# Performance work log

Measured on AMD Instinct MI355X. Metric: run time of the kernel, lower is better.

## Reference

```python
import jax, jax.numpy as jnp
import numpy as np

N = 10000   # nodes
E = 80000   # edges per graph (avg degree 8)
H = 32      # hidden width (hard-coded in module)
VD0 = 2048  # visual_dim for gcn_0
VD1 = 256   # visual_dim // 8 for gcn_b21


def setup_inputs() -> dict:
    key = jax.random.key(0)
    ks = jax.random.split(key, 16)
    rn = lambda k, s, sc=1.0: jax.random.normal(k, s, dtype=jnp.float32) * sc
    return {
        "x": rn(ks[0], (N, 9)),
        "vis0": rn(ks[1], (N, VD0)),
        "vis1": rn(ks[2], (N, VD1)),
        "edge_index0": jax.random.randint(ks[3], (2, E), 0, N),
        "edge_index1": jax.random.randint(ks[4], (2, E), 0, N),
        # input_mlp: Linear(9,32) -> BatchNorm1d(32) (eval) -> PReLU -> Dropout(0) -> Linear(32,32)
        "W_in1": rn(ks[5], (9, H), 0.3), "b_in1": jnp.zeros((H,), jnp.float32),
        "bn_gamma": jnp.ones((H,), jnp.float32), "bn_beta": jnp.zeros((H,), jnp.float32),
        "bn_mean": jnp.zeros((H,), jnp.float32), "bn_var": jnp.ones((H,), jnp.float32),
        "prelu_a": jnp.asarray(0.25, jnp.float32),
        "W_in2": rn(ks[6], (H, H), 0.15), "b_in2": jnp.zeros((H,), jnp.float32),
        "w_node": rn(ks[7], (H, 1), 0.15), "b_node": jnp.zeros((1,), jnp.float32),
        "W_c0": rn(ks[8], (H, H), 0.15), "b_c0": jnp.zeros((H,), jnp.float32),
        "W_c1": rn(ks[9], (H, H), 0.15), "b_c1": jnp.zeros((H,), jnp.float32),
        "w_p0": rn(ks[10], (H, 1), 0.15), "b_p0": jnp.zeros((1,), jnp.float32),
        "w_p1": rn(ks[11], (H, 1), 0.15), "b_p1": jnp.zeros((1,), jnp.float32),
    }


def _cm_cos_conv(h, edge_index, vis, W, b):
    # gather-weight-scatter: w_e = cos(vis[src], vis[dst]); out_i = (sum_e->i w_e * h[src_e]) @ W + b
    src, dst = edge_index[0], edge_index[1]
    vn = vis * jax.lax.rsqrt(jnp.sum(vis * vis, axis=-1, keepdims=True) + 1e-8)
    w = jnp.sum(vn[src] * vn[dst], axis=-1)  # [E] cosine similarity per edge
    agg = jax.ops.segment_sum(h[src] * w[:, None], dst, num_segments=h.shape[0])  # [N,H]
    return agg @ W + b  # conv_activation=None -> identity


def reference(x, vis0, vis1, edge_index0, edge_index1, W_in1, b_in1, bn_gamma, bn_beta, bn_mean, bn_var, prelu_a, W_in2, b_in2, w_node, b_node, W_c0, b_c0, W_c1, b_c1, w_p0, b_p0, w_p1, b_p1):
    h = x @ W_in1 + b_in1
    h = bn_gamma * (h - bn_mean) * jax.lax.rsqrt(bn_var + 1e-5) + bn_beta
    h = jnp.where(h >= 0, h, prelu_a * h)  # PReLU (single shared slope)
    h = h @ W_in2 + b_in2                   # [N,32] shared for graphs 0 and 4
    nodes_scores = (h @ w_node + b_node)[:, 0]
    h0 = _cm_cos_conv(h, edge_index0, vis0, W_c0, b_c0)
    h1 = _cm_cos_conv(h, edge_index1, vis1, W_c1, b_c1)
    s0 = (h0 @ w_p0 + b_p0)[:, 0]
    s1 = (h1 @ w_p1 + b_p1)[:, 0]
    return nodes_scores + s0 + s1
```

## Files before the change

### kernel.cpp

```cpp
#include <hip/hip_runtime.h>

#define N_NODES 10000
#define NE      80000
#define H       32
#define VD0     2048
#define VD1     256

#define EDGE_CAP 32

#define S_BLOCKS 313
#define A_MLP    40
#define A_NC0    2500
#define A_NC1    2500
#define PREP_BLOCKS (S_BLOCKS + A_MLP + A_NC0 + A_NC1)

#define E0_BLOCKS 5000
#define E1_BLOCKS 2500
#define OVF_BLOCKS 16
#define EDGE_BLOCKS (E0_BLOCKS + E1_BLOCKS + OVF_BLOCKS)

__device__ inline int dot4i8(unsigned a, unsigned b, int c) {
#if __has_builtin(__builtin_amdgcn_sdot4)
    return __builtin_amdgcn_sdot4((int)a, (int)b, c, false);
#else
    int s = c;
    s += ((int)(a << 24) >> 24) * ((int)(b << 24) >> 24);
    s += ((int)(a << 16) >> 24) * ((int)(b << 16) >> 24);
    s += ((int)(a <<  8) >> 24) * ((int)(b <<  8) >> 24);
    s += ((int)a >> 24)         * ((int)b >> 24);
    return s;
#endif
}
__device__ inline int dot16i8(uint4 a, uint4 b, int c) {
    c = dot4i8(a.x, b.x, c);
    c = dot4i8(a.y, b.y, c);
    c = dot4i8(a.z, b.z, c);
    c = dot4i8(a.w, b.w, c);
    return c;
}

struct KP {
    const float* x;
    const float* vis0; const float* vis1;
    const int* ei0; const int* ei1;
    const float* W_in1; const float* b_in1;
    const float* bn_gamma; const float* bn_beta;
    const float* bn_mean; const float* bn_var;
    const float* prelu_a;
    const float* W_in2; const float* b_in2;
    const float* w_node; const float* b_node;
    const float* W_c0; const float* b_c0;
    const float* W_c1; const float* b_c1;
    const float* w_p0; const float* b_p0;
    const float* w_p1; const float* b_p1;
    float* out; float* p0w; float* p1w;
    signed char* vn0; signed char* vn1;
    float* s00; float* s01;
    uint2* b0; uint2* b1;
    int2* ovf0; int2* ovf1;
    int* cur0; int* cur1; int* ovfn;
};

template <int VD>
__device__ inline void normconv_q_node(const float* __restrict__ vis,
                                       signed char* __restrict__ vn,
                                       float* __restrict__ s0,
                                       int node, int lane)
{
    const float4* v = (const float4*)(vis + (size_t)node * VD);
    float4 f[VD / 256];
    float acc = 0.f, amax = 0.f;
    #pragma unroll
    for (int it = 0; it < VD / 256; it++) {
        f[it] = v[it * 64 + lane];
        acc += f[it].x * f[it].x + f[it].y * f[it].y
             + f[it].z * f[it].z + f[it].w * f[it].w;
        float m = fmaxf(fmaxf(fabsf(f[it].x), fabsf(f[it].y)),
                        fmaxf(fabsf(f[it].z), fabsf(f[it].w)));
        amax = fmaxf(amax, m);
    }
    #pragma unroll
    for (int o = 32; o; o >>= 1) {
        acc  += __shfl_xor(acc, o);
        amax  = fmaxf(amax, __shfl_xor(amax, o));
    }
    const float inv  = rsqrtf(acc + 1e-8f);
    const float vmax = amax * inv;
    const float k    = vmax > 0.f ? inv * (127.f / vmax) : 0.f;
    if (lane == 0) s0[node] = vmax * (1.f / 127.f);
    uint* o4 = (uint*)(vn + (size_t)node * VD);
    #pragma unroll
    for (int it = 0; it < VD / 256; it++) {
        const int q0 = (int)rintf(f[it].x * k);
        const int q1 = (int)rintf(f[it].y * k);
        const int q2 = (int)rintf(f[it].z * k);
        const int q3 = (int)rintf(f[it].w * k);
        o4[it * 64 + lane] = (unsigned)(q0 & 0xff)
                           | ((unsigned)(q1 & 0xff) << 8)
                           | ((unsigned)(q2 & 0xff) << 16)
                           | ((unsigned)(q3 & 0xff) << 24);
    }
}

__device__ inline void stageA_unit(const KP& p, int u, int t)
{
    if (u < A_MLP) {
        __shared__ float sW1[9 * H];
        __shared__ float sW2[H * H];
        __shared__ float sU0[H], sU1[H], sWn[H];
        __shared__ float sB1[H], sB2[H], sSc[H], sSh[H];
        __shared__ float sC;

        for (int i = t; i < 9 * H; i += 256) sW1[i] = p.W_in1[i];
        for (int i = t; i < H * H; i += 256) sW2[i] = p.W_in2[i];
        if (t < H) {
            sB1[t] = p.b_in1[t];
            sB2[t] = p.b_in2[t];
            float sc = p.bn_gamma[t] * rsqrtf(p.bn_var[t] + 1e-5f);
            sSc[t] = sc;
            sSh[t] = p.bn_beta[t] - p.bn_mean[t] * sc;
            sWn[t] = p.w_node[t];
            float u0 = 0.f, u1 = 0.f;
            for (int j = 0; j < H; j++) {
                u0 += p.W_c0[t * H + j] * p.w_p0[j];
                u1 += p.W_c1[t * H + j] * p.w_p1[j];
            }
            sU0[t] = u0; sU1[t] = u1;
        }
        if (t == 0) {
            float c0 = p.b_p0[0], c1 = p.b_p1[0];
            for (int j = 0; j < H; j++) { c0 += p.b_c0[j] * p.w_p0[j]; c1 += p.b_c1[j] * p.w_p1[j]; }
            sC = c0 + c1 + p.b_node[0];
        }
        __syncthreads();

        const float a = p.prelu_a[0];
        const int n = u * 256 + t;
        if (n < N_NODES) {
            float xi[9];
            #pragma unroll
            for (int i = 0; i < 9; i++) xi[i] = p.x[n * 9 + i];

            float tt[H];
            #pragma unroll
            for (int j = 0; j < H; j++) {
                float s = sB1[j];
                #pragma unroll
                for (int i = 0; i < 9; i++) s += xi[i] * sW1[i * H + j];
                s = s * sSc[j] + sSh[j];
                tt[j] = s >= 0.f ? s : a * s;
            }

            float ns = 0.f, p0 = 0.f, p1 = 0.f;
            #pragma unroll
            for (int k = 0; k < H; k++) {
                float h = sB2[k];
                #pragma unroll
                for (int j = 0; j < H; j++) h += tt[j] * sW2[j * H + k];
                ns += h * sWn[k];
                p0 += h * sU0[k];
                p1 += h * sU1[k];
            }
            p.out[n] = ns + sC;
            p.p0w[n] = p0;
            p.p1w[n] = p1;
        }
    } else if (u < A_MLP + A_NC0) {
        const int node = (u - A_MLP) * 4 + (t >> 6);
        normconv_q_node<VD0>(p.vis0, p.vn0, p.s00, node, t & 63);
    } else {
        const int node = (u - A_MLP - A_NC0) * 4 + (t >> 6);
        normconv_q_node<VD1>(p.vis1, p.vn1, p.s01, node, t & 63);
    }
}

__device__ inline void stageB_edge(const KP& p, int e)
{
    {
        const int s = p.ei0[e];
        const int d = p.ei0[NE + e];
        const int pos = atomicAdd(&p.cur0[d], 1);
        if (pos < EDGE_CAP)
            p.b0[d * EDGE_CAP + pos] = make_uint2((unsigned)(s * VD0), (unsigned)s);
        else
            p.ovf0[atomicAdd(&p.ovfn[0], 1)] = make_int2(d, s);
    }
    {
        const int s = p.ei1[e];
        const int d = p.ei1[NE + e];
        const int pos = atomicAdd(&p.cur1[d], 1);
        if (pos < EDGE_CAP)
            p.b1[d * EDGE_CAP + pos] = make_uint2((unsigned)(s * VD1), (unsigned)s);
        else
            p.ovf1[atomicAdd(&p.ovfn[1], 1)] = make_int2(d, s);
    }
}

__global__ __launch_bounds__(256) void edge4_kernel(KP p)
{
    const int bid  = blockIdx.x;
    const int t    = threadIdx.x;
    const int lane = t & 63;
    const int warp = t >> 6;

    if (bid < E0_BLOCKS) {
        const int phase = bid & 1;
        const int d     = (bid >> 1) * 4 + warp;
        int cnt = p.cur0[d];
        if (cnt <= 0) return;
        cnt = cnt < EDGE_CAP ? cnt : EDGE_CAP;

        const char* base = (const char*)p.vn0;
        const int koffB  = phase * 1024 + lane * 16;
        const uint4 dreg = *(const uint4*)(base + (size_t)d * VD0 + koffB);
        const uint2* eb  = p.b0 + (size_t)d * EDGE_CAP;

        float partial = 0.f;
        int j = 0;
        for (; j + 3 < cnt; j += 4) {
            const uint2 e0 = eb[j], e1 = eb[j + 1], e2 = eb[j + 2], e3 = eb[j + 3];
            const uint4 r0 = *(const uint4*)(base + e0.x + koffB);
            const uint4 r1 = *(const uint4*)(base + e1.x + koffB);
            const uint4 r2 = *(const uint4*)(base + e2.x + koffB);
            const uint4 r3 = *(const uint4*)(base + e3.x + koffB);
            const float w0 = p.p0w[e0.y] * p.s00[e0.y];
            const float w1 = p.p0w[e1.y] * p.s00[e1.y];
            const float w2 = p.p0w[e2.y] * p.s00[e2.y];
            const float w3 = p.p0w[e3.y] * p.s00[e3.y];
            partial += (float)dot16i8(dreg, r0, 0) * w0;
            partial += (float)dot16i8(dreg, r1, 0) * w1;
            partial += (float)dot16i8(dreg, r2, 0) * w2;
            partial += (float)dot16i8(dreg, r3, 0) * w3;
        }
        for (; j < cnt; j++) {
            const uint2 e0 = eb[j];
            const uint4 r0 = *(const uint4*)(base + e0.x + koffB);
            partial += (float)dot16i8(dreg, r0, 0) * (p.p0w[e0.y] * p.s00[e0.y]);
        }
        #pragma unroll
        for (int o = 32; o; o >>= 1) partial += __shfl_down(partial, o);
        if (lane == 0) atomicAdd(&p.out[d], partial * p.s00[d]);
    } else if (bid < E0_BLOCKS + E1_BLOCKS) {
        const int d = (bid - E0_BLOCKS) * 4 + warp;
        int cnt = p.cur1[d];
        if (cnt <= 0) return;
        cnt = cnt < EDGE_CAP ? cnt : EDGE_CAP;

        const char* base = (const char*)p.vn1;
        const int koffB  = lane * 4;
        const unsigned dreg = *(const unsigned*)(base + (size_t)d * VD1 + koffB);
        const uint2* eb  = p.b1 + (size_t)d * EDGE_CAP;

        float partial = 0.f;
        int j = 0;
        for (; j + 3 < cnt; j += 4) {
            const uint2 e0 = eb[j], e1 = eb[j + 1], e2 = eb[j + 2], e3 = eb[j + 3];
            const unsigned r0 = *(const unsigned*)(base + e0.x + koffB);
            const unsigned r1 = *(const unsigned*)(base + e1.x + koffB);
            const unsigned r2 = *(const unsigned*)(base + e2.x + koffB);
            const unsigned r3 = *(const unsigned*)(base + e3.x + koffB);
            const float w0 = p.p1w[e0.y] * p.s01[e0.y];
            const float w1 = p.p1w[e1.y] * p.s01[e1.y];
            const float w2 = p.p1w[e2.y] * p.s01[e2.y];
            const float w3 = p.p1w[e3.y] * p.s01[e3.y];
            partial += (float)dot4i8(dreg, r0, 0) * w0;
            partial += (float)dot4i8(dreg, r1, 0) * w1;
            partial += (float)dot4i8(dreg, r2, 0) * w2;
            partial += (float)dot4i8(dreg, r3, 0) * w3;
        }
        for (; j < cnt; j++) {
            const uint2 e0 = eb[j];
            const unsigned r0 = *(const unsigned*)(base + e0.x + koffB);
            partial += (float)dot4i8(dreg, r0, 0) * (p.p1w[e0.y] * p.s01[e0.y]);
        }
        #pragma unroll
        for (int o = 32; o; o >>= 1) partial += __shfl_down(partial, o);
        if (lane == 0) atomicAdd(&p.out[d], partial * p.s01[d]);
    } else {
        const int wv = (bid - E0_BLOCKS - E1_BLOCKS) * 4 + warp;
        const int n0 = p.ovfn[0];
        for (int i = wv; i < n0; i += OVF_BLOCKS * 4) {
            const int2 ds = p.ovf0[i];
            const uint4* A = (const uint4*)(p.vn0 + (size_t)ds.y * VD0);
            const uint4* B = (const uint4*)(p.vn0 + (size_t)ds.x * VD0);
            int id = 0;
            id = dot16i8(A[lane * 2],     B[lane * 2],     id);
            id = dot16i8(A[lane * 2 + 1], B[lane * 2 + 1], id);
            float acc = (float)id;
            #pragma unroll
            for (int o = 32; o; o >>= 1) acc += __shfl_down(acc, o);
            if (lane == 0)
                atomicAdd(&p.out[ds.x],
                          acc * p.s00[ds.y] * p.s00[ds.x] * p.p0w[ds.y]);
        }
        const int n1 = p.ovfn[1];
        for (int i = wv; i < n1; i += OVF_BLOCKS * 4) {
            const int2 ds = p.ovf1[i];
            const unsigned* A = (const unsigned*)(p.vn1 + (size_t)ds.y * VD1);
            const unsigned* B = (const unsigned*)(p.vn1 + (size_t)ds.x * VD1);
            float acc = (float)dot4i8(A[lane], B[lane], 0);
            #pragma unroll
            for (int o = 32; o; o >>= 1) acc += __shfl_down(acc, o);
            if (lane == 0)
                atomicAdd(&p.out[ds.x],
                          acc * p.s01[ds.y] * p.s01[ds.x] * p.p1w[ds.y]);
        }
    }
}

__global__ __launch_bounds__(256) void prep4_kernel(KP p)
{
    const int b = blockIdx.x, t = threadIdx.x;
    if (b < S_BLOCKS) {
        const int e = b * 256 + t;
        if (e < NE) stageB_edge(p, e);
    } else {
        stageA_unit(p, b - S_BLOCKS, t);
    }
}

template <int VD>
__global__ __launch_bounds__(256) void norm_kernel(const float* __restrict__ vis,
                                                   float* __restrict__ inv)
{
    const int wave = (blockIdx.x * 256 + threadIdx.x) >> 6;
    const int lane = threadIdx.x & 63;
    if (wave >= N_NODES) return;
    const float4* v = (const float4*)(vis + (size_t)wave * VD);
    float acc = 0.f;
    #pragma unroll
    for (int it = 0; it < VD / 256; it++) {
        float4 f = v[lane + it * 64];
        acc += f.x * f.x + f.y * f.y + f.z * f.z + f.w * f.w;
    }
    #pragma unroll
    for (int o = 32; o; o >>= 1) acc += __shfl_down(acc, o);
    if (lane == 0) inv[wave] = rsqrtf(acc + 1e-8f);
}

template <int VD>
__global__ __launch_bounds__(256) void edge_kernel(
    const float* __restrict__ vis, const int* __restrict__ ei,
    const float* __restrict__ inv, const float* __restrict__ pz,
    float* __restrict__ out)
{
    const int wave = (blockIdx.x * 256 + threadIdx.x) >> 6;
    const int lane = threadIdx.x & 63;
    if (wave >= NE) return;
    const int src = ei[wave];
    const int dst = ei[NE + wave];
    const float4* va = (const float4*)(vis + (size_t)src * VD);
    const float4* vb = (const float4*)(vis + (size_t)dst * VD);
    float acc = 0.f;
    #pragma unroll
    for (int it = 0; it < VD / 256; it++) {
        float4 fa = va[lane + it * 64];
        float4 fb = vb[lane + it * 64];
        acc += fa.x * fb.x + fa.y * fb.y + fa.z * fb.z + fa.w * fb.w;
    }
    #pragma unroll
    for (int o = 32; o; o >>= 1) acc += __shfl_down(acc, o);
    if (lane == 0) {
        float w = acc * inv[src] * inv[dst];
        atomicAdd(&out[dst], w * pz[src]);
    }
}

__global__ __launch_bounds__(256) void node_kernel_fb(KP p)
{
    stageA_unit(p, (int)blockIdx.x, (int)threadIdx.x);
}

extern "C" void kernel_launch(void* const* d_in, const int* in_sizes, int n_in,
                              void* d_out, int out_size, void* d_ws, size_t ws_size,
                              hipStream_t stream)
{
    KP hp;
    hp.x        = (const float*)d_in[0];
    hp.vis0     = (const float*)d_in[1];
    hp.vis1     = (const float*)d_in[2];
    hp.ei0      = (const int*)d_in[3];
    hp.ei1      = (const int*)d_in[4];
    hp.W_in1    = (const float*)d_in[5];
    hp.b_in1    = (const float*)d_in[6];
    hp.bn_gamma = (const float*)d_in[7];
    hp.bn_beta  = (const float*)d_in[8];
    hp.bn_mean  = (const float*)d_in[9];
    hp.bn_var   = (const float*)d_in[10];
    hp.prelu_a  = (const float*)d_in[11];
    hp.W_in2    = (const float*)d_in[12];
    hp.b_in2    = (const float*)d_in[13];
    hp.w_node   = (const float*)d_in[14];
    hp.b_node   = (const float*)d_in[15];
    hp.W_c0     = (const float*)d_in[16];
    hp.b_c0     = (const float*)d_in[17];
    hp.W_c1     = (const float*)d_in[18];
    hp.b_c1     = (const float*)d_in[19];
    hp.w_p0     = (const float*)d_in[20];
    hp.b_p0     = (const float*)d_in[21];
    hp.w_p1     = (const float*)d_in[22];
    hp.b_p1     = (const float*)d_in[23];
    hp.out      = (float*)d_out;

    char* ws = (char*)d_ws;
    hp.p0w  = (float*)ws;                  ws += N_NODES * 4;
    hp.p1w  = (float*)ws;                  ws += N_NODES * 4;
    float* inv0 = (float*)ws;              ws += N_NODES * 4;
    float* inv1 = (float*)ws;              ws += N_NODES * 4;
    hp.s00  = (float*)ws;                  ws += N_NODES * 4;
    hp.s01  = (float*)ws;                  ws += N_NODES * 4;
    hp.vn0  = (signed char*)ws;            ws += (size_t)N_NODES * VD0;
    hp.vn1  = (signed char*)ws;            ws += (size_t)N_NODES * VD1;
    hp.b0   = (uint2*)ws;                  ws += (size_t)N_NODES * EDGE_CAP * 8;
    hp.b1   = (uint2*)ws;                  ws += (size_t)N_NODES * EDGE_CAP * 8;
    hp.ovf0 = (int2*)ws;                   ws += (size_t)NE * 8;
    hp.ovf1 = (int2*)ws;                   ws += (size_t)NE * 8;
    hp.cur0 = (int*)ws;                    ws += N_NODES * 4;
    hp.cur1 = (int*)ws;                    ws += N_NODES * 4;
    hp.ovfn = (int*)ws;                    ws += 16;
    const size_t need = (size_t)(ws - (char*)d_ws);

    if (ws_size >= need) {
        hipMemsetAsync(hp.cur0, 0, 2 * N_NODES * sizeof(int) + 16, stream);
        prep4_kernel<<<PREP_BLOCKS, 256, 0, stream>>>(hp);
        edge4_kernel<<<EDGE_BLOCKS, 256, 0, stream>>>(hp);
    } else {
        node_kernel_fb<<<A_MLP, 256, 0, stream>>>(hp);
        norm_kernel<VD0><<<(N_NODES * 64 + 255) / 256, 256, 0, stream>>>(hp.vis0, inv0);
        norm_kernel<VD1><<<(N_NODES * 64 + 255) / 256, 256, 0, stream>>>(hp.vis1, inv1);
        edge_kernel<VD0><<<(NE * 64 + 255) / 256, 256, 0, stream>>>(hp.vis0, hp.ei0, inv0, hp.p0w, hp.out);
        edge_kernel<VD1><<<(NE * 64 + 255) / 256, 256, 0, stream>>>(hp.vis1, hp.ei1, inv1, hp.p1w, hp.out);
    }
}
```

Baseline: 210.3 us.

## Restructure prep kernel: block-per-node vis0 quantization, fold MLP second layer

Quantizing vis0 now uses a full 256-thread block per node, reducing across waves in shared memory, instead of one wave per node looping over eight float4 loads. This aims to raise memory-level parallelism on the largest input read. The block order is changed so the vis0 blocks are scheduled first, and launch bounds now request 8 blocks per CU. The MLP folds W_in2 and its bias into precomputed projection vectors, which removes the per-thread 32x32 matmul. The cost is an extra __syncthreads and a small shared reduction per node.

After: 215.5 us. +2.5%, slower.

```diff
diff --git a/kernel.cpp b/kernel.cpp
--- a/kernel.cpp
+++ b/kernel.cpp
@@ -8,11 +8,11 @@
 
 #define EDGE_CAP 32
 
-#define S_BLOCKS 313
-#define A_MLP    40
-#define A_NC0    2500
-#define A_NC1    2500
-#define PREP_BLOCKS (S_BLOCKS + A_MLP + A_NC0 + A_NC1)
+#define P_NC0   10000
+#define P_NC1   2500
+#define P_SCAT  313
+#define P_MLP   40
+#define PREP_BLOCKS (P_NC0 + P_NC1 + P_SCAT + P_MLP)
 
 #define E0_BLOCKS 5000
 #define E1_BLOCKS 2500
@@ -37,6 +37,15 @@
     c = dot4i8(a.z, b.z, c);
     c = dot4i8(a.w, b.w, c);
     return c;
+}
+
+__device__ inline unsigned packq4(float4 f, float k) {
+    const int q0 = (int)rintf(f.x * k);
+    const int q1 = (int)rintf(f.y * k);
+    const int q2 = (int)rintf(f.z * k);
+    const int q3 = (int)rintf(f.w * k);
+    return (unsigned)(q0 & 0xff) | ((unsigned)(q1 & 0xff) << 8)
+         | ((unsigned)(q2 & 0xff) << 16) | ((unsigned)(q3 & 0xff) << 24);
 }
 
 struct KP {
@@ -61,117 +70,129 @@
     int* cur0; int* cur1; int* ovfn;
 };
 
-template <int VD>
-__device__ inline void normconv_q_node(const float* __restrict__ vis,
-                                       signed char* __restrict__ vn,
-                                       float* __restrict__ s0,
-                                       int node, int lane)
-{
-    const float4* v = (const float4*)(vis + (size_t)node * VD);
-    float4 f[VD / 256];
-    float acc = 0.f, amax = 0.f;
-    #pragma unroll
-    for (int it = 0; it < VD / 256; it++) {
-        f[it] = v[it * 64 + lane];
-        acc += f[it].x * f[it].x + f[it].y * f[it].y
-             + f[it].z * f[it].z + f[it].w * f[it].w;
-        float m = fmaxf(fmaxf(fabsf(f[it].x), fabsf(f[it].y)),
-                        fmaxf(fabsf(f[it].z), fabsf(f[it].w)));
-        amax = fmaxf(amax, m);
-    }
+__device__ inline void nc0_block(const KP& p, int node, int t)
+{
+    const float4* v = (const float4*)(p.vis0 + (size_t)node * VD0);
+    const float4 fa = v[t];
+    const float4 fb = v[t + 256];
+    float acc  = fa.x * fa.x + fa.y * fa.y + fa.z * fa.z + fa.w * fa.w
+               + fb.x * fb.x + fb.y * fb.y + fb.z * fb.z + fb.w * fb.w;
+    float amax = fmaxf(fmaxf(fmaxf(fabsf(fa.x), fabsf(fa.y)),
+                             fmaxf(fabsf(fa.z), fabsf(fa.w))),
+                       fmaxf(fmaxf(fabsf(fb.x), fabsf(fb.y)),
+                             fmaxf(fabsf(fb.z), fabsf(fb.w))));
     #pragma unroll
     for (int o = 32; o; o >>= 1) {
-        acc  += __shfl_xor(acc, o);
-        amax  = fmaxf(amax, __shfl_xor(amax, o));
-    }
+        acc += __shfl_xor(acc, o);
+        amax = fmaxf(amax, __shfl_xor(amax, o));
+    }
+    __shared__ float red[8];
+    const int lane = t & 63, warp = t >> 6;
+    if (lane == 0) { red[warp] = acc; red[4 + warp] = amax; }
+    __syncthreads();
+    acc  = red[0] + red[1] + red[2] + red[3];
+    amax = fmaxf(fmaxf(red[4], red[5]), fmaxf(red[6], red[7]));
+
     const float inv  = rsqrtf(acc + 1e-8f);
     const float vmax = amax * inv;
     const float k    = vmax > 0.f ? inv * (127.f / vmax) : 0.f;
-    if (lane == 0) s0[node] = vmax * (1.f / 127.f);
-    uint* o4 = (uint*)(vn + (size_t)node * VD);
-    #pragma unroll
-    for (int it = 0; it < VD / 256; it++) {
-        const int q0 = (int)rintf(f[it].x * k);
-        const int q1 = (int)rintf(f[it].y * k);
-        const int q2 = (int)rintf(f[it].z * k);
-        const int q3 = (int)rintf(f[it].w * k);
-        o4[it * 64 + lane] = (unsigned)(q0 & 0xff)
-                           | ((unsigned)(q1 & 0xff) << 8)
-                           | ((unsigned)(q2 & 0xff) << 16)
-                           | ((unsigned)(q3 & 0xff) << 24);
-    }
-}
-
-__device__ inline void stageA_unit(const KP& p, int u, int t)
-{
-    if (u < A_MLP) {
-        __shared__ float sW1[9 * H];
-        __shared__ float sW2[H * H];
-        __shared__ float sU0[H], sU1[H], sWn[H];
-        __shared__ float sB1[H], sB2[H], sSc[H], sSh[H];
-        __shared__ float sC;
-
-        for (int i = t; i < 9 * H; i += 256) sW1[i] = p.W_in1[i];
-        for (int i = t; i < H * H; i += 256) sW2[i] = p.W_in2[i];
-        if (t < H) {
-            sB1[t] = p.b_in1[t];
-            sB2[t] = p.b_in2[t];
-            float sc = p.bn_gamma[t] * rsqrtf(p.bn_var[t] + 1e-5f);
-            sSc[t] = sc;
-            sSh[t] = p.bn_beta[t] - p.bn_mean[t] * sc;
-            sWn[t] = p.w_node[t];
-            float u0 = 0.f, u1 = 0.f;
-            for (int j = 0; j < H; j++) {
-                u0 += p.W_c0[t * H + j] * p.w_p0[j];
-                u1 += p.W_c1[t * H + j] * p.w_p1[j];
-            }
-            sU0[t] = u0; sU1[t] = u1;
-        }
-        if (t == 0) {
-            float c0 = p.b_p0[0], c1 = p.b_p1[0];
-            for (int j = 0; j < H; j++) { c0 += p.b_c0[j] * p.w_p0[j]; c1 += p.b_c1[j] * p.w_p1[j]; }
-            sC = c0 + c1 + p.b_node[0];
-        }
-        __syncthreads();
-
-        const float a = p.prelu_a[0];
-        const int n = u * 256 + t;
-        if (n < N_NODES) {
-            float xi[9];
-            #pragma unroll
-            for (int i = 0; i < 9; i++) xi[i] = p.x[n * 9 + i];
-
-            float tt[H];
-            #pragma unroll
-            for (int j = 0; j < H; j++) {
-                float s = sB1[j];
-                #pragma unroll
-                for (int i = 0; i < 9; i++) s += xi[i] * sW1[i * H + j];
-                s = s * sSc[j] + sSh[j];
-                tt[j] = s >= 0.f ? s : a * s;
-            }
-
-            float ns = 0.f, p0 = 0.f, p1 = 0.f;
-            #pragma unroll
-            for (int k = 0; k < H; k++) {
-                float h = sB2[k];
-                #pragma unroll
-                for (int j = 0; j < H; j++) h += tt[j] * sW2[j * H + k];
-                ns += h * sWn[k];
-                p0 += h * sU0[k];
-                p1 += h * sU1[k];
-            }
-            p.out[n] = ns + sC;
-            p.p0w[n] = p0;
-            p.p1w[n] = p1;
-        }
-    } else if (u < A_MLP + A_NC0) {
-        const int node = (u - A_MLP) * 4 + (t >> 6);
-        normconv_q_node<VD0>(p.vis0, p.vn0, p.s00, node, t & 63);
-    } else {
-        const int node = (u - A_MLP - A_NC0) * 4 + (t >> 6);
-        normconv_q_node<VD1>(p.vis1, p.vn1, p.s01, node, t & 63);
-    }
+    if (t == 0) p.s00[node] = vmax * (1.f / 127.f);
+    uint* o4 = (uint*)(p.vn0 + (size_t)node * VD0);
+    o4[t]       = packq4(fa, k);
+    o4[t + 256] = packq4(fb, k);
+}
+
+__device__ inline void nc1_wave(const KP& p, int node, int lane)
+{
+    const float4* v = (const float4*)(p.vis1 + (size_t)node * VD1);
+    const float4 f = v[lane];
+    float acc  = f.x * f.x + f.y * f.y + f.z * f.z + f.w * f.w;
+    float amax = fmaxf(fmaxf(fabsf(f.x), fabsf(f.y)),
+                       fmaxf(fabsf(f.z), fabsf(f.w)));
+    #pragma unroll
+    for (int o = 32; o; o >>= 1) {
+        acc += __shfl_xor(acc, o);
+        amax = fmaxf(amax, __shfl_xor(amax, o));
+    }
+    const float inv  = rsqrtf(acc + 1e-8f);
+    const float vmax = amax * inv;
+    const float k    = vmax > 0.f ? inv * (127.f / vmax) : 0.f;
+    if (lane == 0) p.s01[node] = vmax * (1.f / 127.f);
+    uint* o4 = (uint*)(p.vn1 + (size_t)node * VD1);
+    o4[lane] = packq4(f, k);
+}
+
+__device__ inline void mlp_block(const KP& p, int u, int t)
+{
+    __shared__ float sW1[9 * H];
+    __shared__ float sV0[H], sV1[H], sVn[H];
+    __shared__ float sB1[H], sSc[H], sSh[H];
+    __shared__ float sU0[H], sU1[H], sWn[H], sB2[H];
+    __shared__ float sCn, sC0, sC1;
+
+    for (int i = t; i < 9 * H; i += 256) sW1[i] = p.W_in1[i];
+    if (t < H) {
+        sB1[t] = p.b_in1[t];
+        sB2[t] = p.b_in2[t];
+        float sc = p.bn_gamma[t] * rsqrtf(p.bn_var[t] + 1e-5f);
+        sSc[t] = sc;
+        sSh[t] = p.bn_beta[t] - p.bn_mean[t] * sc;
+        sWn[t] = p.w_node[t];
+        float u0 = 0.f, u1 = 0.f;
+        for (int j = 0; j < H; j++) {
+            u0 += p.W_c0[t * H + j] * p.w_p0[j];
+            u1 += p.W_c1[t * H + j] * p.w_p1[j];
+        }
+        sU0[t] = u0; sU1[t] = u1;
+    }
+    __syncthreads();
+    if (t < H) {
+        float v0 = 0.f, v1 = 0.f, vn = 0.f;
+        for (int k = 0; k < H; k++) {
+            const float w2 = p.W_in2[t * H + k];
+            v0 += w2 * sU0[k];
+            v1 += w2 * sU1[k];
+            vn += w2 * sWn[k];
+        }
+        sV0[t] = v0; sV1[t] = v1; sVn[t] = vn;
+    }
+    if (t == 0) {
+        float c0 = p.b_p0[0], c1 = p.b_p1[0];
+        for (int j = 0; j < H; j++) { c0 += p.b_c0[j] * p.w_p0[j]; c1 += p.b_c1[j] * p.w_p1[j]; }
+        float d0 = 0.f, d1 = 0.f, dn = 0.f;
+        for (int k = 0; k < H; k++) {
+            d0 += sB2[k] * sU0[k];
+            d1 += sB2[k] * sU1[k];
+            dn += sB2[k] * sWn[k];
+        }
+        sC0 = d0; sC1 = d1;
+        sCn = dn + p.b_node[0] + c0 + c1;
+    }
+    __syncthreads();
+
+    const float a = p.prelu_a[0];
+    const int n = u * 256 + t;
+    if (n >= N_NODES) return;
+
+    float xi[9];
+    #pragma unroll
+    for (int i = 0; i < 9; i++) xi[i] = p.x[n * 9 + i];
+
+    float ns = 0.f, p0 = 0.f, p1 = 0.f;
+    #pragma unroll
+    for (int j = 0; j < H; j++) {
+        float s = sB1[j];
+        #pragma unroll
+        for (int i = 0; i < 9; i++) s += xi[i] * sW1[i * H + j];
+        s = s * sSc[j] + sSh[j];
+        const float tt = s >= 0.f ? s : a * s;
+        ns += tt * sVn[j];
+        p0 += tt * sV0[j];
+        p1 += tt * sV1[j];
+    }
+    p.out[n] = ns + sCn;
+    p.p0w[n] = p0 + sC0;
+    p.p1w[n] = p1 + sC1;
 }
 
 __device__ inline void stageB_edge(const KP& p, int e)
@@ -193,6 +214,22 @@
             p.b1[d * EDGE_CAP + pos] = make_uint2((unsigned)(s * VD1), (unsigned)s);
         else
             p.ovf1[atomicAdd(&p.ovfn[1], 1)] = make_int2(d, s);
+    }
+}
+
+__global__ __launch_bounds__(256, 8) void prep5_kernel(KP p)
+{
+    const int b = blockIdx.x, t = threadIdx.x;
+    if (b < P_NC0) {
+        nc0_block(p, b, t);
+    } else if (b < P_NC0 + P_NC1) {
+        const int node = (b - P_NC0) * 4 + (t >> 6);
+        nc1_wave(p, node, t & 63);
+    } else if (b < P_NC0 + P_NC1 + P_SCAT) {
+        const int e = (b - P_NC0 - P_NC1) * 256 + t;
+        if (e < NE) stageB_edge(p, e);
+    } else {
+        mlp_block(p, b - P_NC0 - P_NC1 - P_SCAT, t);
     }
 }
 
@@ -308,17 +345,6 @@
     }
 }
 
-__global__ __launch_bounds__(256) void prep4_kernel(KP p)
-{
-    const int b = blockIdx.x, t = threadIdx.x;
-    if (b < S_BLOCKS) {
-        const int e = b * 256 + t;
-        if (e < NE) stageB_edge(p, e);
-    } else {
-        stageA_unit(p, b - S_BLOCKS, t);
-    }
-}
-
 template <int VD>
 __global__ __launch_bounds__(256) void norm_kernel(const float* __restrict__ vis,
                                                    float* __restrict__ inv)
@@ -368,7 +394,7 @@
 
 __global__ __launch_bounds__(256) void node_kernel_fb(KP p)
 {
-    stageA_unit(p, (int)blockIdx.x, (int)threadIdx.x);
+    mlp_block(p, (int)blockIdx.x, (int)threadIdx.x);
 }
 
 extern "C" void kernel_launch(void* const* d_in, const int* in_sizes, int n_in,
@@ -422,10 +448,10 @@
 
     if (ws_size >= need) {
         hipMemsetAsync(hp.cur0, 0, 2 * N_NODES * sizeof(int) + 16, stream);
-        prep4_kernel<<<PREP_BLOCKS, 256, 0, stream>>>(hp);
+        prep5_kernel<<<PREP_BLOCKS, 256, 0, stream>>>(hp);
         edge4_kernel<<<EDGE_BLOCKS, 256, 0, stream>>>(hp);
     } else {
-        node_kernel_fb<<<A_MLP, 256, 0, stream>>>(hp);
+        node_kernel_fb<<<P_MLP, 256, 0, stream>>>(hp);
         norm_kernel<VD0><<<(N_NODES * 64 + 255) / 256, 256, 0, stream>>>(hp.vis0, inv0);
         norm_kernel<VD1><<<(N_NODES * 64 + 255) / 256, 256, 0, stream>>>(hp.vis1, inv1);
         edge_kernel<VD0><<<(NE * 64 + 255) / 256, 256, 0, stream>>>(hp.vis0, hp.ei0, inv0, hp.p0w, hp.out);
```
